# Kernel tuning notes

Hardware: AMD Instinct MI355X
Metric: run time of the kernel (lower is better)

The kernel has to match this reference:

```python
import jax, jax.numpy as jnp
import numpy as np

EPS = 1e-08


def setup_inputs() -> dict:
    key = jax.random.key(0)
    k1, k2 = jax.random.split(key)
    x = jax.random.normal(k1, (8192, 4096), dtype=jnp.float32)
    # xavier-uniform-ish init for weight (faithful scale; exact init irrelevant to math)
    limit = float(np.sqrt(6.0 / (4096 + 4096)))
    weight = jax.random.uniform(k2, (4096, 4096), dtype=jnp.float32, minval=-limit, maxval=limit)
    mask = jnp.ones((4096, 4096), dtype=jnp.float32)
    bias = jnp.zeros((4096,), dtype=jnp.float32)
    return {"x": x, "weight": weight, "mask": mask, "bias": bias}


def reference(x, weight, mask, bias):
    # masked weights
    mw = weight * mask  # [out, in]
    aw = jnp.abs(mw)
    # per-call global stats (training mode, adaptive threshold)
    scale = aw.mean() + EPS
    threshold = jnp.std(aw, ddof=1) * 0.5  # torch .std() is unbiased
    # ternary {-1, 0, +1} then rescale
    tern = jnp.where(mw > threshold, 1.0, 0.0) + jnp.where(mw < -threshold, -1.0, 0.0)
    tw = tern * scale
    # F.linear: x @ W^T + b
    return jnp.einsum("bi,oi->bo", x, tw) + bias
```

## Files before the change

kernel.cpp:

```cpp
#include <hip/hip_runtime.h>
#include <hip/hip_bf16.h>
#include <stdint.h>

#define M_DIM 8192
#define N_DIM 4096
#define K_DIM 4096
#define NW (N_DIM * K_DIM)

typedef __bf16 bf16x8 __attribute__((ext_vector_type(8)));
typedef float  floatx4 __attribute__((ext_vector_type(4)));
typedef unsigned short u16;
typedef unsigned int   u32;

__global__ void zero_stats(double* S) {
    if (threadIdx.x < 2) S[threadIdx.x] = 0.0;
}

__global__ void reduce_moments(const float* __restrict__ w,
                               const float* __restrict__ msk,
                               double* __restrict__ S) {
    const int nv = NW / 4;
    const int stride = gridDim.x * blockDim.x;
    int idx = blockIdx.x * blockDim.x + threadIdx.x;
    float s1 = 0.f, s2 = 0.f;
    const float4* w4 = (const float4*)w;
    const float4* m4 = (const float4*)msk;
    for (int i = idx; i < nv; i += stride) {
        float4 a = w4[i];
        float4 b = m4[i];
        float p0 = fabsf(a.x * b.x), p1 = fabsf(a.y * b.y);
        float p2 = fabsf(a.z * b.z), p3 = fabsf(a.w * b.w);
        s1 += p0 + p1 + p2 + p3;
        s2 += p0 * p0 + p1 * p1 + p2 * p2 + p3 * p3;
    }
    double d1 = (double)s1, d2 = (double)s2;
    #pragma unroll
    for (int off = 32; off > 0; off >>= 1) {
        d1 += __shfl_down(d1, off);
        d2 += __shfl_down(d2, off);
    }
    __shared__ double sh[8];
    int lane = threadIdx.x & 63;
    int wv = threadIdx.x >> 6;
    if (lane == 0) { sh[wv] = d1; sh[wv + 4] = d2; }
    __syncthreads();
    if (threadIdx.x == 0) {
        atomicAdd(&S[0], sh[0] + sh[1] + sh[2] + sh[3]);
        atomicAdd(&S[1], sh[4] + sh[5] + sh[6] + sh[7]);
    }
}

__global__ void finalize_stats(const double* __restrict__ S, float* __restrict__ st) {
    if (threadIdx.x == 0) {
        const double n = (double)NW;
        double s1 = S[0], s2 = S[1];
        double mean = s1 / n;
        double var = (s2 - s1 * s1 / n) / (n - 1.0);
        st[0] = (float)(mean + 1e-8);
        st[1] = (float)(0.5 * sqrt(var));
    }
}

__global__ void ternarize(const float* __restrict__ w, const float* __restrict__ msk,
                          const float* __restrict__ st, u16* __restrict__ tw) {
    const float thr = st[1];
    const int i = (blockIdx.x * blockDim.x + threadIdx.x) * 8;
    float4 a0 = *(const float4*)(w + i);
    float4 a1 = *(const float4*)(w + i + 4);
    float4 b0 = *(const float4*)(msk + i);
    float4 b1 = *(const float4*)(msk + i + 4);
    float p[8] = {a0.x * b0.x, a0.y * b0.y, a0.z * b0.z, a0.w * b0.w,
                  a1.x * b1.x, a1.y * b1.y, a1.z * b1.z, a1.w * b1.w};
    union { u16 u[8]; uint4 v; } r;
    #pragma unroll
    for (int j = 0; j < 8; ++j)
        r.u[j] = p[j] > thr ? (u16)0x3F80 : (p[j] < -thr ? (u16)0xBF80 : (u16)0);
    *(uint4*)(tw + i) = r.v;
}

__device__ __forceinline__ u16 f2bf(float f) {
    u32 u = __float_as_uint(f);
    u += 0x7FFFu + ((u >> 16) & 1u);
    return (u16)(u >> 16);
}

__global__ void cvt_x(const float* __restrict__ x, u16* __restrict__ y) {
    const int i = (blockIdx.x * blockDim.x + threadIdx.x) * 8;
    float4 a0 = *(const float4*)(x + i);
    float4 a1 = *(const float4*)(x + i + 4);
    union { u16 u[8]; uint4 v; } r;
    r.u[0] = f2bf(a0.x); r.u[1] = f2bf(a0.y); r.u[2] = f2bf(a0.z); r.u[3] = f2bf(a0.w);
    r.u[4] = f2bf(a1.x); r.u[5] = f2bf(a1.y); r.u[6] = f2bf(a1.z); r.u[7] = f2bf(a1.w);
    *(uint4*)(y + i) = r.v;
}

__device__ __forceinline__ void gld_lds16(const __bf16* g, __bf16* l) {
    __builtin_amdgcn_global_load_lds(
        (__attribute__((address_space(1))) void*)g,
        (__attribute__((address_space(3))) void*)l, 16, 0, 0);
}

__global__ __launch_bounds__(256) void gemm_tern(
        const __bf16* __restrict__ A, const __bf16* __restrict__ B,
        const float* __restrict__ bias, const float* __restrict__ st,
        float* __restrict__ C) {
    __shared__ __bf16 As[128 * 32];
    __shared__ __bf16 Bs[128 * 32];

    const int t = threadIdx.x;
    const int lane = t & 63;
    const int wv = t >> 6;
    const int wm = (wv >> 1) * 64;
    const int wn = (wv & 1) * 64;
    const int bm = blockIdx.y * 128;
    const int bn = blockIdx.x * 128;

    const int r  = t >> 2;
    const int kk = (t & 3) * 8;
    const __bf16* ga0 = A + (size_t)(bm + r) * K_DIM + kk;
    const __bf16* ga1 = A + (size_t)(bm + 64 + r) * K_DIM + kk;
    const __bf16* gb0 = B + (size_t)(bn + r) * K_DIM + kk;
    const __bf16* gb1 = B + (size_t)(bn + 64 + r) * K_DIM + kk;
    __bf16* la0 = As + t * 8;
    __bf16* la1 = As + 2048 + t * 8;
    __bf16* lb0 = Bs + t * 8;
    __bf16* lb1 = Bs + 2048 + t * 8;

    floatx4 acc[4][4] = {};

    const int mrow = lane & 15;
    const int kc = (lane >> 4) * 8;

    for (int k0 = 0; k0 < K_DIM; k0 += 32) {
        __syncthreads();
        gld_lds16(ga0 + k0, la0);
        gld_lds16(ga1 + k0, la1);
        gld_lds16(gb0 + k0, lb0);
        gld_lds16(gb1 + k0, lb1);
        __syncthreads();

        bf16x8 af[4], bfr[4];
        #pragma unroll
        for (int i = 0; i < 4; ++i) {
            af[i]  = *(const bf16x8*)(As + (wm + i * 16 + mrow) * 32 + kc);
            bfr[i] = *(const bf16x8*)(Bs + (wn + i * 16 + mrow) * 32 + kc);
        }
        #pragma unroll
        for (int im = 0; im < 4; ++im)
            #pragma unroll
            for (int in = 0; in < 4; ++in)
                acc[im][in] = __builtin_amdgcn_mfma_f32_16x16x32_bf16(
                    af[im], bfr[in], acc[im][in], 0, 0, 0);
    }

    const float scale = st[0];
    const int rbase = bm + wm + ((lane >> 4) << 2);
    const int cbase = bn + wn + (lane & 15);
    #pragma unroll
    for (int in = 0; in < 4; ++in) {
        const int col = cbase + in * 16;
        const float bv = bias[col];
        #pragma unroll
        for (int im = 0; im < 4; ++im) {
            const int row = rbase + im * 16;
            #pragma unroll
            for (int rg = 0; rg < 4; ++rg)
                C[(size_t)(row + rg) * N_DIM + col] = acc[im][in][rg] * scale + bv;
        }
    }
}

extern "C" void kernel_launch(void* const* d_in, const int* in_sizes, int n_in,
                              void* d_out, int out_size, void* d_ws, size_t ws_size,
                              hipStream_t stream) {
    const float* x    = (const float*)d_in[0];
    const float* w    = (const float*)d_in[1];
    const float* msk  = (const float*)d_in[2];
    const float* bias = (const float*)d_in[3];
    float* out = (float*)d_out;

    char* ws = (char*)d_ws;
    double* S   = (double*)ws;
    float*  st  = (float*)(ws + 64);
    u16*    tern = (u16*)(ws + 256);
    u16*    xbf  = (u16*)(ws + 256 + (size_t)NW * 2);

    zero_stats<<<1, 64, 0, stream>>>(S);
    reduce_moments<<<1024, 256, 0, stream>>>(w, msk, S);
    finalize_stats<<<1, 64, 0, stream>>>(S, st);
    ternarize<<<NW / (256 * 8), 256, 0, stream>>>(w, msk, st, tern);
    cvt_x<<<(M_DIM * K_DIM) / (256 * 8), 256, 0, stream>>>(x, xbf);

    dim3 grid(N_DIM / 128, M_DIM / 128);
    gemm_tern<<<grid, 256, 0, stream>>>((const __bf16*)xbf, (const __bf16*)tern,
                                        bias, st, out);
}
```

Baseline: 646.5 us.

## Rewrite GEMM as 256x256 pipelined tile, fuse prep kernels, drop atomics

The GEMM moves from 128x128 tiles with 4 waves and two barriers per k-step to 256x256 tiles with 8 waves, K=64 steps, and double-buffered LDS staging through global_load_lds. It uses swizzled LDS addressing, phased MFMA with s_setprio, and vmcnt-based waits. The moment reduction now writes per-block partials that a single block reduces, which removes the zero kernel and the double atomics. Ternarize and bf16 conversion of x are merged into one launch. The goal is higher operand reuse, less global traffic and fewer launches, at the cost of 128KB LDS, heavy register use and fragile hand-written synchronisation. The partials buffer shares its workspace offset with the ternary weights, which relies on finalize running before tern_cvt overwrites that region.

After: 537.6 us. -16.8%, faster.

```diff
diff --git a/kernel.cpp b/kernel.cpp
--- a/kernel.cpp
+++ b/kernel.cpp
@@ -1,24 +1,20 @@
 #include <hip/hip_runtime.h>
-#include <hip/hip_bf16.h>
 #include <stdint.h>
 
 #define M_DIM 8192
 #define N_DIM 4096
 #define K_DIM 4096
 #define NW (N_DIM * K_DIM)
+#define RM_BLOCKS 2048
 
 typedef __bf16 bf16x8 __attribute__((ext_vector_type(8)));
 typedef float  floatx4 __attribute__((ext_vector_type(4)));
 typedef unsigned short u16;
 typedef unsigned int   u32;
 
-__global__ void zero_stats(double* S) {
-    if (threadIdx.x < 2) S[threadIdx.x] = 0.0;
-}
-
 __global__ void reduce_moments(const float* __restrict__ w,
                                const float* __restrict__ msk,
-                               double* __restrict__ S) {
+                               double* __restrict__ part) {
     const int nv = NW / 4;
     const int stride = gridDim.x * blockDim.x;
     int idx = blockIdx.x * blockDim.x + threadIdx.x;
@@ -45,37 +41,36 @@
     if (lane == 0) { sh[wv] = d1; sh[wv + 4] = d2; }
     __syncthreads();
     if (threadIdx.x == 0) {
-        atomicAdd(&S[0], sh[0] + sh[1] + sh[2] + sh[3]);
-        atomicAdd(&S[1], sh[4] + sh[5] + sh[6] + sh[7]);
-    }
-}
-
-__global__ void finalize_stats(const double* __restrict__ S, float* __restrict__ st) {
+        part[blockIdx.x]             = sh[0] + sh[1] + sh[2] + sh[3];
+        part[RM_BLOCKS + blockIdx.x] = sh[4] + sh[5] + sh[6] + sh[7];
+    }
+}
+
+__global__ void finalize_stats(const double* __restrict__ part, float* __restrict__ st) {
+    double s1 = 0.0, s2 = 0.0;
+    for (int i = threadIdx.x; i < RM_BLOCKS; i += 256) {
+        s1 += part[i];
+        s2 += part[RM_BLOCKS + i];
+    }
+    #pragma unroll
+    for (int off = 32; off > 0; off >>= 1) {
+        s1 += __shfl_down(s1, off);
+        s2 += __shfl_down(s2, off);
+    }
+    __shared__ double sh[8];
+    int lane = threadIdx.x & 63;
+    int wv = threadIdx.x >> 6;
+    if (lane == 0) { sh[wv] = s1; sh[wv + 4] = s2; }
+    __syncthreads();
     if (threadIdx.x == 0) {
+        double S1 = sh[0] + sh[1] + sh[2] + sh[3];
+        double S2 = sh[4] + sh[5] + sh[6] + sh[7];
         const double n = (double)NW;
-        double s1 = S[0], s2 = S[1];
-        double mean = s1 / n;
-        double var = (s2 - s1 * s1 / n) / (n - 1.0);
+        double mean = S1 / n;
+        double var = (S2 - S1 * S1 / n) / (n - 1.0);
         st[0] = (float)(mean + 1e-8);
         st[1] = (float)(0.5 * sqrt(var));
     }
-}
-
-__global__ void ternarize(const float* __restrict__ w, const float* __restrict__ msk,
-                          const float* __restrict__ st, u16* __restrict__ tw) {
-    const float thr = st[1];
-    const int i = (blockIdx.x * blockDim.x + threadIdx.x) * 8;
-    float4 a0 = *(const float4*)(w + i);
-    float4 a1 = *(const float4*)(w + i + 4);
-    float4 b0 = *(const float4*)(msk + i);
-    float4 b1 = *(const float4*)(msk + i + 4);
-    float p[8] = {a0.x * b0.x, a0.y * b0.y, a0.z * b0.z, a0.w * b0.w,
-                  a1.x * b1.x, a1.y * b1.y, a1.z * b1.z, a1.w * b1.w};
-    union { u16 u[8]; uint4 v; } r;
-    #pragma unroll
-    for (int j = 0; j < 8; ++j)
-        r.u[j] = p[j] > thr ? (u16)0x3F80 : (p[j] < -thr ? (u16)0xBF80 : (u16)0);
-    *(uint4*)(tw + i) = r.v;
 }
 
 __device__ __forceinline__ u16 f2bf(float f) {
@@ -84,88 +79,177 @@
     return (u16)(u >> 16);
 }
 
-__global__ void cvt_x(const float* __restrict__ x, u16* __restrict__ y) {
-    const int i = (blockIdx.x * blockDim.x + threadIdx.x) * 8;
-    float4 a0 = *(const float4*)(x + i);
-    float4 a1 = *(const float4*)(x + i + 4);
-    union { u16 u[8]; uint4 v; } r;
-    r.u[0] = f2bf(a0.x); r.u[1] = f2bf(a0.y); r.u[2] = f2bf(a0.z); r.u[3] = f2bf(a0.w);
-    r.u[4] = f2bf(a1.x); r.u[5] = f2bf(a1.y); r.u[6] = f2bf(a1.z); r.u[7] = f2bf(a1.w);
-    *(uint4*)(y + i) = r.v;
-}
-
-__device__ __forceinline__ void gld_lds16(const __bf16* g, __bf16* l) {
+__global__ void tern_cvt(const float* __restrict__ w, const float* __restrict__ msk,
+                         const float* __restrict__ st, u16* __restrict__ tw,
+                         const float* __restrict__ x, u16* __restrict__ xbf) {
+    const int b = blockIdx.x;
+    if (b < NW / 2048) {
+        const float thr = st[1];
+        const int i = (b * 256 + threadIdx.x) * 8;
+        float4 a0 = *(const float4*)(w + i);
+        float4 a1 = *(const float4*)(w + i + 4);
+        float4 b0 = *(const float4*)(msk + i);
+        float4 b1 = *(const float4*)(msk + i + 4);
+        float p[8] = {a0.x * b0.x, a0.y * b0.y, a0.z * b0.z, a0.w * b0.w,
+                      a1.x * b1.x, a1.y * b1.y, a1.z * b1.z, a1.w * b1.w};
+        union { u16 u[8]; uint4 v; } r;
+        #pragma unroll
+        for (int j = 0; j < 8; ++j)
+            r.u[j] = p[j] > thr ? (u16)0x3F80 : (p[j] < -thr ? (u16)0xBF80 : (u16)0);
+        *(uint4*)(tw + i) = r.v;
+    } else {
+        const int i = ((b - NW / 2048) * 256 + threadIdx.x) * 8;
+        float4 a0 = *(const float4*)(x + i);
+        float4 a1 = *(const float4*)(x + i + 4);
+        union { u16 u[8]; uint4 v; } r;
+        r.u[0] = f2bf(a0.x); r.u[1] = f2bf(a0.y); r.u[2] = f2bf(a0.z); r.u[3] = f2bf(a0.w);
+        r.u[4] = f2bf(a1.x); r.u[5] = f2bf(a1.y); r.u[6] = f2bf(a1.z); r.u[7] = f2bf(a1.w);
+        *(uint4*)(xbf + i) = r.v;
+    }
+}
+
+__device__ __forceinline__ void gld16(const __bf16* g, __bf16* l) {
     __builtin_amdgcn_global_load_lds(
         (__attribute__((address_space(1))) void*)g,
         (__attribute__((address_space(3))) void*)l, 16, 0, 0);
 }
 
-__global__ __launch_bounds__(256) void gemm_tern(
+
+#define BARRIER __builtin_amdgcn_s_barrier()
+#define LGK0    asm volatile("s_waitcnt lgkmcnt(0)" ::: "memory")
+#define VMC4    asm volatile("s_waitcnt vmcnt(4)" ::: "memory")
+
+#define STAGE_A(ktn, dst)                                           \
+    gld16(gA[0] + (ktn) * 64, sh + (dst) + (0 * 8 + wv) * 512);     \
+    gld16(gA[1] + (ktn) * 64, sh + (dst) + (1 * 8 + wv) * 512);     \
+    gld16(gA[2] + (ktn) * 64, sh + (dst) + (2 * 8 + wv) * 512);     \
+    gld16(gA[3] + (ktn) * 64, sh + (dst) + (3 * 8 + wv) * 512);
+
+#define STAGE_BH(ktn, dst, h)                                                   \
+    gld16(gB[(h) * 2 + 0] + (ktn) * 64, sh + (dst) + ((h) * 16 + wv * 2 + 0) * 512); \
+    gld16(gB[(h) * 2 + 1] + (ktn) * 64, sh + (dst) + ((h) * 16 + wv * 2 + 1) * 512);
+
+#define PHASE(pidx, aCur, STAGE_CODE)                                           \
+    {                                                                           \
+        bf16x8 af[2][2];                                                        \
+        _Pragma("unroll")                                                       \
+        for (int mi = 0; mi < 2; ++mi)                                          \
+            _Pragma("unroll")                                                   \
+            for (int ks = 0; ks < 2; ++ks)                                      \
+                af[mi][ks] = *(const bf16x8*)(sh + (aCur) +                     \
+                    ((rsA + (pidx) * 2 + mi) * 2 + ks) * 512 + laneElem);       \
+        STAGE_CODE                                                              \
+        BARRIER;                                                                \
+        LGK0;                                                                   \
+        __builtin_amdgcn_s_setprio(1);                                          \
+        _Pragma("unroll")                                                       \
+        for (int mi = 0; mi < 2; ++mi)                                          \
+            _Pragma("unroll")                                                   \
+            for (int ni = 0; ni < 4; ++ni)                                      \
+                _Pragma("unroll")                                               \
+                for (int ks = 0; ks < 2; ++ks)                                  \
+                    acc[(pidx) * 2 + mi][ni] =                                  \
+                        __builtin_amdgcn_mfma_f32_16x16x32_bf16(                \
+                            af[mi][ks], bfr[ni][ks], acc[(pidx) * 2 + mi][ni],  \
+                            0, 0, 0);                                           \
+        __builtin_amdgcn_s_setprio(0);                                          \
+    }
+
+#define TILE(P, kt)                                                             \
+    {                                                                           \
+        const int aCur = (P) * 16384;                                           \
+        const int aNxt = ((P) ^ 1) * 16384;                                     \
+        const int bCur = 32768 + (P) * 16384;                                   \
+        const int kt1 = ((kt) + 1) & 63;                                        \
+        const int kt2 = ((kt) + 2) & 63;                                        \
+        _Pragma("unroll")                                                       \
+        for (int ni = 0; ni < 4; ++ni)                                          \
+            _Pragma("unroll")                                                   \
+            for (int ks = 0; ks < 2; ++ks)                                      \
+                bfr[ni][ks] = *(const bf16x8*)(sh + bCur +                      \
+                    ((rsB + ni) * 2 + ks) * 512 + laneElem);                    \
+        PHASE(0, aCur, STAGE_A(kt1, aNxt))                                      \
+        BARRIER;                                                                \
+        PHASE(1, aCur, STAGE_BH(kt2, bCur, 0))                                  \
+        BARRIER;                                                                \
+        PHASE(2, aCur, STAGE_BH(kt2, bCur, 1))                                  \
+        BARRIER;                                                                \
+        PHASE(3, aCur, ;)                                                       \
+        VMC4;                                                                   \
+        BARRIER;                                                                \
+    }
+
+__global__ __launch_bounds__(512, 2) void gemm_tern(
         const __bf16* __restrict__ A, const __bf16* __restrict__ B,
         const float* __restrict__ bias, const float* __restrict__ st,
         float* __restrict__ C) {
-    __shared__ __bf16 As[128 * 32];
-    __shared__ __bf16 Bs[128 * 32];
+    __shared__ __bf16 sh[65536];
 
     const int t = threadIdx.x;
     const int lane = t & 63;
     const int wv = t >> 6;
-    const int wm = (wv >> 1) * 64;
-    const int wn = (wv & 1) * 64;
-    const int bm = blockIdx.y * 128;
-    const int bn = blockIdx.x * 128;
-
-    const int r  = t >> 2;
-    const int kk = (t & 3) * 8;
-    const __bf16* ga0 = A + (size_t)(bm + r) * K_DIM + kk;
-    const __bf16* ga1 = A + (size_t)(bm + 64 + r) * K_DIM + kk;
-    const __bf16* gb0 = B + (size_t)(bn + r) * K_DIM + kk;
-    const __bf16* gb1 = B + (size_t)(bn + 64 + r) * K_DIM + kk;
-    __bf16* la0 = As + t * 8;
-    __bf16* la1 = As + 2048 + t * 8;
-    __bf16* lb0 = Bs + t * 8;
-    __bf16* lb1 = Bs + 2048 + t * 8;
-
-    floatx4 acc[4][4] = {};
-
-    const int mrow = lane & 15;
-    const int kc = (lane >> 4) * 8;
-
-    for (int k0 = 0; k0 < K_DIM; k0 += 32) {
-        __syncthreads();
-        gld_lds16(ga0 + k0, la0);
-        gld_lds16(ga1 + k0, la1);
-        gld_lds16(gb0 + k0, lb0);
-        gld_lds16(gb1 + k0, lb1);
-        __syncthreads();
-
-        bf16x8 af[4], bfr[4];
-        #pragma unroll
-        for (int i = 0; i < 4; ++i) {
-            af[i]  = *(const bf16x8*)(As + (wm + i * 16 + mrow) * 32 + kc);
-            bfr[i] = *(const bf16x8*)(Bs + (wn + i * 16 + mrow) * 32 + kc);
-        }
-        #pragma unroll
-        for (int im = 0; im < 4; ++im)
-            #pragma unroll
-            for (int in = 0; in < 4; ++in)
-                acc[im][in] = __builtin_amdgcn_mfma_f32_16x16x32_bf16(
-                    af[im], bfr[in], acc[im][in], 0, 0, 0);
+    const int wm = (wv >> 2) * 128;
+    const int wn = (wv & 3) * 64;
+    const int bm = blockIdx.y * 256;
+    const int bn = blockIdx.x * 256;
+
+    const int laneElem = ((lane & 15) << 5) +
+                         (((lane >> 4) << 3) ^ ((lane & 8) << 1));
+    const int rsA = wm >> 4;
+    const int rsB = wn >> 4;
+
+    const int lp = lane ^ ((lane & 32) >> 4);
+    const int srow = lp >> 2;
+    const int scol = (lp & 3) * 8;
+
+    const __bf16* gA[4];
+    #pragma unroll
+    for (int i = 0; i < 4; ++i) {
+        int stA = i * 8 + wv;
+        gA[i] = A + (size_t)(bm + (stA >> 1) * 16 + srow) * K_DIM +
+                (stA & 1) * 32 + scol;
+    }
+    const __bf16* gB[4];
+    #pragma unroll
+    for (int j = 0; j < 2; ++j) {
+        int st0 = wv * 2 + j;
+        gB[j] = B + (size_t)(bn + (st0 >> 1) * 16 + srow) * K_DIM +
+                (st0 & 1) * 32 + scol;
+        int st1 = 16 + wv * 2 + j;
+        gB[2 + j] = B + (size_t)(bn + (st1 >> 1) * 16 + srow) * K_DIM +
+                    (st1 & 1) * 32 + scol;
+    }
+
+    floatx4 acc[8][4] = {};
+    bf16x8 bfr[4][2];
+
+    STAGE_A(0, 0)
+    STAGE_BH(0, 32768, 0)
+    STAGE_BH(0, 32768, 1)
+    STAGE_BH(1, 32768 + 16384, 0)
+    STAGE_BH(1, 32768 + 16384, 1)
+    VMC4;
+    BARRIER;
+
+    #pragma unroll 1
+    for (int t2 = 0; t2 < 64; t2 += 2) {
+        TILE(0, t2)
+        TILE(1, t2 + 1)
     }
 
     const float scale = st[0];
     const int rbase = bm + wm + ((lane >> 4) << 2);
     const int cbase = bn + wn + (lane & 15);
     #pragma unroll
-    for (int in = 0; in < 4; ++in) {
-        const int col = cbase + in * 16;
+    for (int ni = 0; ni < 4; ++ni) {
+        const int col = cbase + ni * 16;
         const float bv = bias[col];
         #pragma unroll
-        for (int im = 0; im < 4; ++im) {
-            const int row = rbase + im * 16;
+        for (int mi = 0; mi < 8; ++mi) {
+            const int row = rbase + mi * 16;
             #pragma unroll
             for (int rg = 0; rg < 4; ++rg)
-                C[(size_t)(row + rg) * N_DIM + col] = acc[im][in][rg] * scale + bv;
+                C[(size_t)(row + rg) * N_DIM + col] = acc[mi][ni][rg] * scale + bv;
         }
     }
 }
@@ -180,18 +264,17 @@
     float* out = (float*)d_out;
 
     char* ws = (char*)d_ws;
-    double* S   = (double*)ws;
-    float*  st  = (float*)(ws + 64);
+    float*  st   = (float*)(ws + 64);
+    double* part = (double*)(ws + 256);
     u16*    tern = (u16*)(ws + 256);
     u16*    xbf  = (u16*)(ws + 256 + (size_t)NW * 2);
 
-    zero_stats<<<1, 64, 0, stream>>>(S);
-    reduce_moments<<<1024, 256, 0, stream>>>(w, msk, S);
-    finalize_stats<<<1, 64, 0, stream>>>(S, st);
-    ternarize<<<NW / (256 * 8), 256, 0, stream>>>(w, msk, st, tern);
-    cvt_x<<<(M_DIM * K_DIM) / (256 * 8), 256, 0, stream>>>(x, xbf);
-
-    dim3 grid(N_DIM / 128, M_DIM / 128);
-    gemm_tern<<<grid, 256, 0, stream>>>((const __bf16*)xbf, (const __bf16*)tern,
+    reduce_moments<<<RM_BLOCKS, 256, 0, stream>>>(w, msk, part);
+    finalize_stats<<<1, 256, 0, stream>>>(part, st);
+    tern_cvt<<<NW / 2048 + (M_DIM * K_DIM) / 2048, 256, 0, stream>>>(
+        w, msk, st, tern, x, xbf);
+
+    dim3 grid(N_DIM / 256, M_DIM / 256);
+    gemm_tern<<<grid, 512, 0, stream>>>((const __bf16*)xbf, (const __bf16*)tern,
                                         bias, st, out);
 }
```
